# Kernel optimization log

Hardware: AMD Instinct MI355X
Metric: run time of the kernel (lower is better)

The kernel has to match this reference:

```python
import jax, jax.numpy as jnp
import numpy as np

N = 100000
E = 1600000
D = 128

def _degrees(idx, n):
    d = jax.ops.segment_sum(jnp.ones(idx.shape[0], jnp.float32), idx, num_segments=n)
    return jnp.clip(d, 1.0)

def _gconv(feat, src, dst, W, b, residual, act):
    n = feat.shape[0]
    norm_out = _degrees(src, n) ** -0.5            # [N] out-degree norm
    h = feat * norm_out[:, None]                   # scale src features
    msgs = h[src]                                  # gather [E, D]
    agg = jax.ops.segment_sum(msgs, dst, num_segments=n)  # scatter-sum [N, D]
    rst = agg @ W.T + b                            # dense linear
    norm_in = _degrees(dst, n) ** -0.5             # [N] in-degree norm
    rst = rst * norm_in[:, None]
    if residual:
        rst = rst + feat                           # identity residual (in==out)
    if act:
        rst = jax.nn.relu(rst)
    return rst

def setup_inputs() -> dict:
    key = jax.random.key(0)
    ks = jax.random.split(key, 10)
    feat = jax.random.normal(ks[0], (N, D), jnp.float32)
    src = jax.random.randint(ks[1], (E,), 0, N)
    dst = jax.random.randint(ks[2], (E,), 0, N)
    s = 1.0 / np.sqrt(D)
    W1 = jax.random.uniform(ks[3], (D, D), jnp.float32, -s, s)
    b1 = jax.random.uniform(ks[4], (D,), jnp.float32, -s, s)
    W2 = jax.random.uniform(ks[5], (D, D), jnp.float32, -s, s)
    b2 = jax.random.uniform(ks[6], (D,), jnp.float32, -s, s)
    W3 = jax.random.uniform(ks[7], (D, D), jnp.float32, -s, s)
    b3 = jax.random.uniform(ks[8], (D,), jnp.float32, -s, s)
    return {"feat": feat, "src": src, "dst": dst,
            "W1": W1, "b1": b1, "W2": W2, "b2": b2, "W3": W3, "b3": b3}

def reference(feat, src, dst, W1, b1, W2, b2, W3, b3):
    # 3-layer GCN, dropout=0, norm=None, encoding=False:
    # layers 0,1: residual + relu; layer 2: no residual, no activation
    h = _gconv(feat, src, dst, W1, b1, residual=True, act=True)
    h = _gconv(h, src, dst, W2, b2, residual=True, act=True)
    h = _gconv(h, src, dst, W3, b3, residual=False, act=False)
    return h
```

## Files before the change

### kernel.cpp

```cpp
#include <hip/hip_runtime.h>

#define NN 100000
#define EE 1600000
#define DD 128
#define NB 512
#define CAP 4608
#define CHUNK 8192

typedef __attribute__((ext_vector_type(8))) short short8v;
typedef __attribute__((ext_vector_type(4))) float f32x4;
typedef __attribute__((ext_vector_type(8))) unsigned short ushort8v;

#define LROW 136

static __device__ __forceinline__ unsigned short f2bf(float x) {
  unsigned u = __builtin_bit_cast(unsigned, x);
  return (unsigned short)((u + 0x7FFFu + ((u >> 16) & 1u)) >> 16);
}
static __device__ __forceinline__ float bf2f(unsigned short u) {
  return __builtin_bit_cast(float, (unsigned)u << 16);
}

__global__ __launch_bounds__(512) void initcur_k(int* __restrict__ cur_d,
                                                 int* __restrict__ cur_s) {
  int t = threadIdx.x;
  cur_d[t] = t * CAP;
  cur_s[t] = t * CAP;
}

__global__ __launch_bounds__(256) void split_k(const int* __restrict__ src,
                                               const int* __restrict__ dst,
                                               int* __restrict__ cur_d,
                                               int* __restrict__ cur_s,
                                               unsigned* __restrict__ tmp_d,
                                               unsigned char* __restrict__ tmp_s) {
  __shared__ int hd[NB], hs[NB], bd[NB], bs[NB];
  int t = threadIdx.x;
  int base = blockIdx.x * CHUNK;
  int end = base + CHUNK < EE ? base + CHUNK : EE;
  for (int b = t; b < NB; b += 256) { hd[b] = 0; hs[b] = 0; }
  __syncthreads();
  for (int i = base + t; i < end; i += 256) {
    atomicAdd(&hd[dst[i] >> 8], 1);
    atomicAdd(&hs[src[i] >> 8], 1);
  }
  __syncthreads();
  for (int b = t; b < NB; b += 256) {
    bd[b] = hd[b] ? atomicAdd(&cur_d[b], hd[b]) : 0;
    bs[b] = hs[b] ? atomicAdd(&cur_s[b], hs[b]) : 0;
    hd[b] = 0;
    hs[b] = 0;
  }
  __syncthreads();
  for (int i = base + t; i < end; i += 256) {
    int s = src[i];
    int d = dst[i];
    int bin = d >> 8;
    int r = atomicAdd(&hd[bin], 1);
    int pos = bd[bin] + r;
    if (pos < (bin + 1) * CAP) tmp_d[pos] = ((unsigned)(d & 255) << 17) | (unsigned)s;
    bin = s >> 8;
    r = atomicAdd(&hs[bin], 1);
    pos = bs[bin] + r;
    if (pos < (bin + 1) * CAP) tmp_s[pos] = (unsigned char)(s & 255);
  }
}

__global__ __launch_bounds__(512) void scan512_k(const int* __restrict__ cur_d,
                                                 int* __restrict__ dstart) {
  __shared__ int lds[512];
  int t = threadIdx.x;
  int v = cur_d[t] - t * CAP;
  v = v < CAP ? v : CAP;
  lds[t] = v;
  __syncthreads();
  int run = v;
  for (int off = 1; off < 512; off <<= 1) {
    int y = (t >= off) ? lds[t - off] : 0;
    __syncthreads();
    run += y;
    lds[t] = run;
    __syncthreads();
  }
  dstart[t] = run - v;
}

__global__ __launch_bounds__(256) void bucket_dst_k(const unsigned* __restrict__ tmp_d,
                                                    const int* __restrict__ cur_d,
                                                    const int* __restrict__ dstart,
                                                    int* __restrict__ csr,
                                                    int* __restrict__ row_s,
                                                    int* __restrict__ row_e,
                                                    float* __restrict__ norm_in) {
  __shared__ unsigned stage[CAP];
  __shared__ int h[256], sc[256], rk[256];
  int b = blockIdx.x;
  int t = threadIdx.x;
  int cnt = cur_d[b] - b * CAP;
  cnt = cnt < CAP ? cnt : CAP;
  int ds = dstart[b];
  for (int i = t; i < cnt; i += 256) stage[i] = tmp_d[b * CAP + i];
  h[t] = 0;
  __syncthreads();
  for (int i = t; i < cnt; i += 256) atomicAdd(&h[stage[i] >> 17], 1);
  __syncthreads();
  int v = h[t];
  sc[t] = v;
  __syncthreads();
  int run = v;
  for (int off = 1; off < 256; off <<= 1) {
    int y = (t >= off) ? sc[t - off] : 0;
    __syncthreads();
    run += y;
    sc[t] = run;
    __syncthreads();
  }
  int excl = run - v;
  int n = b * 256 + t;
  if (n < NN) {
    row_s[n] = ds + excl;
    row_e[n] = ds + excl + v;
    norm_in[n] = rsqrtf((float)(v > 1 ? v : 1));
  }
  rk[t] = excl;
  __syncthreads();
  for (int i = t; i < cnt; i += 256) {
    unsigned w = stage[i];
    int r = atomicAdd(&rk[w >> 17], 1);
    csr[ds + r] = (int)(w & 0x1FFFFu);
  }
}

__global__ __launch_bounds__(256) void bucket_src_k(const unsigned char* __restrict__ tmp_s,
                                                    const int* __restrict__ cur_s,
                                                    float* __restrict__ norm_out) {
  __shared__ int h[256];
  int b = blockIdx.x;
  int t = threadIdx.x;
  int cnt = cur_s[b] - b * CAP;
  cnt = cnt < CAP ? cnt : CAP;
  h[t] = 0;
  __syncthreads();
  const unsigned char* p = tmp_s + b * CAP;
  for (int i = t; i < cnt; i += 256) atomicAdd(&h[p[i]], 1);
  __syncthreads();
  int n = b * 256 + t;
  if (n < NN) norm_out[n] = rsqrtf((float)(h[t] > 1 ? h[t] : 1));
}

__global__ __launch_bounds__(256) void bconv_k(const float* __restrict__ w,
                                               unsigned short* __restrict__ o) {
  int i = blockIdx.x * 256 + threadIdx.x;
  float4 v = *reinterpret_cast<const float4*>(w + i * 4);
  ushort4 pk = make_ushort4(f2bf(v.x), f2bf(v.y), f2bf(v.z), f2bf(v.w));
  *reinterpret_cast<ushort4*>(o + i * 4) = pk;
}

__global__ __launch_bounds__(256) void layer_k(const unsigned short* __restrict__ h,
                                               const int* __restrict__ csr,
                                               const int* __restrict__ row_s,
                                               const int* __restrict__ row_e,
                                               const float* __restrict__ nsrc,
                                               const unsigned short* __restrict__ Wb,
                                               const float* __restrict__ bias,
                                               const float* __restrict__ nin,
                                               const float* __restrict__ residf,
                                               const unsigned short* __restrict__ residb,
                                               float* __restrict__ outf,
                                               unsigned short* __restrict__ outb,
                                               int mode) {
  __shared__ unsigned short tile[16 * LROW];
  int t = threadIdx.x;
  int n16 = t >> 4;
  int c = t & 15;
  int node = blockIdx.x * 16 + n16;

  int e0 = row_s[node];
  int e1 = row_e[node];
  float acc[8] = {0.f, 0.f, 0.f, 0.f, 0.f, 0.f, 0.f, 0.f};
  int e = e0;
  for (; e + 2 <= e1; e += 2) {
    int s0 = csr[e];
    int s1 = csr[e + 1];
    float n0 = nsrc[s0];
    float n1 = nsrc[s1];
    ushort8v u = *reinterpret_cast<const ushort8v*>(h + (size_t)s0 * DD + c * 8);
    ushort8v v = *reinterpret_cast<const ushort8v*>(h + (size_t)s1 * DD + c * 8);
#pragma unroll
    for (int i = 0; i < 8; ++i) acc[i] += bf2f(u[i]) * n0 + bf2f(v[i]) * n1;
  }
  if (e < e1) {
    int s0 = csr[e];
    float n0 = nsrc[s0];
    ushort8v u = *reinterpret_cast<const ushort8v*>(h + (size_t)s0 * DD + c * 8);
#pragma unroll
    for (int i = 0; i < 8; ++i) acc[i] += bf2f(u[i]) * n0;
  }
  ushort8v o;
#pragma unroll
  for (int i = 0; i < 8; ++i) o[i] = f2bf(acc[i]);
  *reinterpret_cast<ushort8v*>(&tile[n16 * LROW + c * 8]) = o;
  __syncthreads();

  int wid = t >> 6;
  int lane = t & 63;
  int l15 = lane & 15;
  int kgrp = lane >> 4;

  const unsigned short* bp = &tile[l15 * LROW + kgrp * 8];
  short8v b0 = *reinterpret_cast<const short8v*>(bp);
  short8v b1 = *reinterpret_cast<const short8v*>(bp + 32);
  short8v b2 = *reinterpret_cast<const short8v*>(bp + 64);
  short8v b3 = *reinterpret_cast<const short8v*>(bp + 96);

  int epnode = blockIdx.x * 16 + l15;
  float ninv = nin[epnode];

#pragma unroll
  for (int q = 0; q < 2; ++q) {
    int ct = wid * 2 + q;
    const unsigned short* wp = Wb + (size_t)(ct * 16 + l15) * DD + kgrp * 8;
    short8v w0 = *reinterpret_cast<const short8v*>(wp);
    short8v w1 = *reinterpret_cast<const short8v*>(wp + 32);
    short8v w2 = *reinterpret_cast<const short8v*>(wp + 64);
    short8v w3 = *reinterpret_cast<const short8v*>(wp + 96);
    f32x4 cacc = {0.f, 0.f, 0.f, 0.f};
    cacc = __builtin_amdgcn_mfma_f32_16x16x32_bf16(w0, b0, cacc, 0, 0, 0);
    cacc = __builtin_amdgcn_mfma_f32_16x16x32_bf16(w1, b1, cacc, 0, 0, 0);
    cacc = __builtin_amdgcn_mfma_f32_16x16x32_bf16(w2, b2, cacc, 0, 0, 0);
    cacc = __builtin_amdgcn_mfma_f32_16x16x32_bf16(w3, b3, cacc, 0, 0, 0);

    int j = ct * 16 + kgrp * 4;
    float4 bj = *reinterpret_cast<const float4*>(bias + j);
    size_t idx = (size_t)epnode * DD + j;
    float4 v;
    v.x = (cacc[0] + bj.x) * ninv;
    v.y = (cacc[1] + bj.y) * ninv;
    v.z = (cacc[2] + bj.z) * ninv;
    v.w = (cacc[3] + bj.w) * ninv;
    if (mode == 1) {
      float4 rs = *reinterpret_cast<const float4*>(residf + idx);
      v.x = fmaxf(v.x + rs.x, 0.f);
      v.y = fmaxf(v.y + rs.y, 0.f);
      v.z = fmaxf(v.z + rs.z, 0.f);
      v.w = fmaxf(v.w + rs.w, 0.f);
      ushort4 hn = make_ushort4(f2bf(v.x), f2bf(v.y), f2bf(v.z), f2bf(v.w));
      *reinterpret_cast<ushort4*>(outb + idx) = hn;
    } else if (mode == 3) {
      ushort4 rs = *reinterpret_cast<const ushort4*>(residb + idx);
      v.x = fmaxf(v.x + bf2f(rs.x), 0.f);
      v.y = fmaxf(v.y + bf2f(rs.y), 0.f);
      v.z = fmaxf(v.z + bf2f(rs.z), 0.f);
      v.w = fmaxf(v.w + bf2f(rs.w), 0.f);
      ushort4 hn = make_ushort4(f2bf(v.x), f2bf(v.y), f2bf(v.z), f2bf(v.w));
      *reinterpret_cast<ushort4*>(outb + idx) = hn;
    } else {
      *reinterpret_cast<float4*>(outf + idx) = v;
    }
  }
}

extern "C" void kernel_launch(void* const* d_in, const int* in_sizes, int n_in,
                              void* d_out, int out_size, void* d_ws, size_t ws_size,
                              hipStream_t stream) {
  const float* feat = (const float*)d_in[0];
  const int* src = (const int*)d_in[1];
  const int* dst = (const int*)d_in[2];
  const float* W1 = (const float*)d_in[3];
  const float* b1 = (const float*)d_in[4];
  const float* W2 = (const float*)d_in[5];
  const float* b2 = (const float*)d_in[6];
  const float* W3 = (const float*)d_in[7];
  const float* b3 = (const float*)d_in[8];
  float* out = (float*)d_out;

  int* row_s = (int*)d_ws;
  int* row_e = row_s + NN;
  float* norm_out = (float*)(row_e + NN);
  float* norm_in = norm_out + NN;
  int* cur_d = (int*)(norm_in + NN);
  int* cur_s = cur_d + NB;
  int* dstart = cur_s + NB;
  int* pad = dstart + NB;
  unsigned short* Wbf = (unsigned short*)pad;
  int* csr = (int*)(Wbf + 3 * 16384);
  unsigned short* vb1 = (unsigned short*)(csr + EE);
  unsigned short* vb2 = vb1 + (size_t)NN * DD;

  unsigned* tmp_d = (unsigned*)d_out;
  unsigned char* tmp_s = (unsigned char*)d_out + (size_t)NB * CAP * 4;

  initcur_k<<<1, 512, 0, stream>>>(cur_d, cur_s);
  split_k<<<(EE + CHUNK - 1) / CHUNK, 256, 0, stream>>>(src, dst, cur_d, cur_s, tmp_d, tmp_s);
  scan512_k<<<1, 512, 0, stream>>>(cur_d, dstart);
  bucket_dst_k<<<NB, 256, 0, stream>>>(tmp_d, cur_d, dstart, csr, row_s, row_e, norm_in);
  bucket_src_k<<<NB, 256, 0, stream>>>(tmp_s, cur_s, norm_out);

  bconv_k<<<16, 256, 0, stream>>>(W1, Wbf);
  bconv_k<<<16, 256, 0, stream>>>(W2, Wbf + 16384);
  bconv_k<<<16, 256, 0, stream>>>(W3, Wbf + 32768);
  bconv_k<<<12500, 256, 0, stream>>>(feat, vb1);

  layer_k<<<6250, 256, 0, stream>>>(vb1, csr, row_s, row_e, norm_out, Wbf, b1,
                                    norm_in, feat, nullptr, nullptr, vb2, 1);
  layer_k<<<6250, 256, 0, stream>>>(vb2, csr, row_s, row_e, norm_out, Wbf + 16384, b2,
                                    norm_in, nullptr, vb2, nullptr, vb1, 3);
  layer_k<<<6250, 256, 0, stream>>>(vb1, csr, row_s, row_e, norm_out, Wbf + 32768, b3,
                                    norm_in, nullptr, nullptr, out, nullptr, 0);
}
```

Baseline: 349.2 us.

## Split fused layer into XCD-sliced column aggregation and separate MFMA GEMM

Replaces the fused gather+GEMM layer kernel with two kernels. The first aggregates neighbour features one 16-column slice at a time. Each block reads its XCD id and takes work from a per-slice atomic counter, so each XCD mostly gathers one 3.2MB column slice of h, which should stay resident in that XCD's L2. The second is a standalone bf16 MFMA GEMM over a materialized aggregate buffer with the fused epilogue. This adds a full N×D bf16 write and read of the aggregate per layer, extra launches and atomic scheduling, and gathers that are now 8-byte rather than 16-byte per lane.

```diff
diff --git a/kernel.cpp b/kernel.cpp
--- a/kernel.cpp
+++ b/kernel.cpp
@@ -6,13 +6,12 @@
 #define NB 512
 #define CAP 4608
 #define CHUNK 8192
+#define NCHUNK 1563
 
 typedef __attribute__((ext_vector_type(8))) short short8v;
 typedef __attribute__((ext_vector_type(4))) float f32x4;
 typedef __attribute__((ext_vector_type(8))) unsigned short ushort8v;
 
-#define LROW 136
-
 static __device__ __forceinline__ unsigned short f2bf(float x) {
   unsigned u = __builtin_bit_cast(unsigned, x);
   return (unsigned short)((u + 0x7FFFu + ((u >> 16) & 1u)) >> 16);
@@ -22,10 +21,12 @@
 }
 
 __global__ __launch_bounds__(512) void initcur_k(int* __restrict__ cur_d,
-                                                 int* __restrict__ cur_s) {
+                                                 int* __restrict__ cur_s,
+                                                 int* __restrict__ scur) {
   int t = threadIdx.x;
   cur_d[t] = t * CAP;
   cur_s[t] = t * CAP;
+  if (t < 32) scur[t] = 0;
 }
 
 __global__ __launch_bounds__(256) void split_k(const int* __restrict__ src,
@@ -156,11 +157,68 @@
   *reinterpret_cast<ushort4*>(o + i * 4) = pk;
 }
 
-__global__ __launch_bounds__(256) void layer_k(const unsigned short* __restrict__ h,
-                                               const int* __restrict__ csr,
-                                               const int* __restrict__ row_s,
-                                               const int* __restrict__ row_e,
-                                               const float* __restrict__ nsrc,
+__global__ __launch_bounds__(256) void sliceagg_k(const unsigned short* __restrict__ h,
+                                                  const int* __restrict__ csr,
+                                                  const int* __restrict__ row_s,
+                                                  const int* __restrict__ row_e,
+                                                  const float* __restrict__ nsrc,
+                                                  int* __restrict__ scur,
+                                                  unsigned short* __restrict__ agg) {
+  __shared__ int pick_sh;
+  if (threadIdx.x == 0) {
+    unsigned xcd;
+    asm volatile("s_getreg_b32 %0, hwreg(HW_REG_XCC_ID)" : "=s"(xcd));
+    xcd &= 7u;
+    int pick = -1;
+    for (int off = 0; off < 8; ++off) {
+      int s = (int)((xcd + off) & 7u);
+      int c = atomicAdd(&scur[s], 1);
+      if (c < NCHUNK) { pick = (s << 16) | c; break; }
+    }
+    pick_sh = pick;
+  }
+  __syncthreads();
+  int pick = pick_sh;
+  if (pick < 0) return;
+  int slice = pick >> 16;
+  int chunk = pick & 0xFFFF;
+
+  int node = chunk * 64 + (threadIdx.x >> 2);
+  if (node >= NN) return;
+  int l4 = threadIdx.x & 3;
+  int colbase = slice * 16 + l4 * 4;
+
+  int e0 = row_s[node];
+  int e1 = row_e[node];
+  float a0 = 0.f, a1 = 0.f, a2 = 0.f, a3 = 0.f;
+  const unsigned short* hb = h + colbase;
+  int e = e0;
+  for (; e + 2 <= e1; e += 2) {
+    int s0 = csr[e];
+    int s1 = csr[e + 1];
+    float n0 = nsrc[s0];
+    float n1 = nsrc[s1];
+    ushort4 u = *reinterpret_cast<const ushort4*>(hb + (size_t)s0 * DD);
+    ushort4 v = *reinterpret_cast<const ushort4*>(hb + (size_t)s1 * DD);
+    a0 += bf2f(u.x) * n0 + bf2f(v.x) * n1;
+    a1 += bf2f(u.y) * n0 + bf2f(v.y) * n1;
+    a2 += bf2f(u.z) * n0 + bf2f(v.z) * n1;
+    a3 += bf2f(u.w) * n0 + bf2f(v.w) * n1;
+  }
+  if (e < e1) {
+    int s0 = csr[e];
+    float n0 = nsrc[s0];
+    ushort4 u = *reinterpret_cast<const ushort4*>(hb + (size_t)s0 * DD);
+    a0 += bf2f(u.x) * n0;
+    a1 += bf2f(u.y) * n0;
+    a2 += bf2f(u.z) * n0;
+    a3 += bf2f(u.w) * n0;
+  }
+  ushort4 o = make_ushort4(f2bf(a0), f2bf(a1), f2bf(a2), f2bf(a3));
+  *reinterpret_cast<ushort4*>(agg + (size_t)node * DD + colbase) = o;
+}
+
+__global__ __launch_bounds__(256) void gemm2_k(const unsigned short* __restrict__ A,
                                                const unsigned short* __restrict__ Wb,
                                                const float* __restrict__ bias,
                                                const float* __restrict__ nin,
@@ -169,93 +227,61 @@
                                                float* __restrict__ outf,
                                                unsigned short* __restrict__ outb,
                                                int mode) {
-  __shared__ unsigned short tile[16 * LROW];
-  int t = threadIdx.x;
-  int n16 = t >> 4;
-  int c = t & 15;
-  int node = blockIdx.x * 16 + n16;
-
-  int e0 = row_s[node];
-  int e1 = row_e[node];
-  float acc[8] = {0.f, 0.f, 0.f, 0.f, 0.f, 0.f, 0.f, 0.f};
-  int e = e0;
-  for (; e + 2 <= e1; e += 2) {
-    int s0 = csr[e];
-    int s1 = csr[e + 1];
-    float n0 = nsrc[s0];
-    float n1 = nsrc[s1];
-    ushort8v u = *reinterpret_cast<const ushort8v*>(h + (size_t)s0 * DD + c * 8);
-    ushort8v v = *reinterpret_cast<const ushort8v*>(h + (size_t)s1 * DD + c * 8);
-#pragma unroll
-    for (int i = 0; i < 8; ++i) acc[i] += bf2f(u[i]) * n0 + bf2f(v[i]) * n1;
-  }
-  if (e < e1) {
-    int s0 = csr[e];
-    float n0 = nsrc[s0];
-    ushort8v u = *reinterpret_cast<const ushort8v*>(h + (size_t)s0 * DD + c * 8);
-#pragma unroll
-    for (int i = 0; i < 8; ++i) acc[i] += bf2f(u[i]) * n0;
-  }
-  ushort8v o;
-#pragma unroll
-  for (int i = 0; i < 8; ++i) o[i] = f2bf(acc[i]);
-  *reinterpret_cast<ushort8v*>(&tile[n16 * LROW + c * 8]) = o;
-  __syncthreads();
-
-  int wid = t >> 6;
-  int lane = t & 63;
+  int wid = threadIdx.x >> 6;
+  int lane = threadIdx.x & 63;
   int l15 = lane & 15;
   int kgrp = lane >> 4;
-
-  const unsigned short* bp = &tile[l15 * LROW + kgrp * 8];
+  int node = blockIdx.x * 64 + wid * 16 + l15;
+  int nodec = node < NN ? node : NN - 1;
+
+  const unsigned short* bp = A + (size_t)nodec * DD + kgrp * 8;
   short8v b0 = *reinterpret_cast<const short8v*>(bp);
   short8v b1 = *reinterpret_cast<const short8v*>(bp + 32);
   short8v b2 = *reinterpret_cast<const short8v*>(bp + 64);
   short8v b3 = *reinterpret_cast<const short8v*>(bp + 96);
 
-  int epnode = blockIdx.x * 16 + l15;
-  float ninv = nin[epnode];
-
-#pragma unroll
-  for (int q = 0; q < 2; ++q) {
-    int ct = wid * 2 + q;
+  float ninv = nin[nodec];
+
+  for (int ct = 0; ct < 8; ++ct) {
     const unsigned short* wp = Wb + (size_t)(ct * 16 + l15) * DD + kgrp * 8;
     short8v w0 = *reinterpret_cast<const short8v*>(wp);
     short8v w1 = *reinterpret_cast<const short8v*>(wp + 32);
     short8v w2 = *reinterpret_cast<const short8v*>(wp + 64);
     short8v w3 = *reinterpret_cast<const short8v*>(wp + 96);
-    f32x4 cacc = {0.f, 0.f, 0.f, 0.f};
-    cacc = __builtin_amdgcn_mfma_f32_16x16x32_bf16(w0, b0, cacc, 0, 0, 0);
-    cacc = __builtin_amdgcn_mfma_f32_16x16x32_bf16(w1, b1, cacc, 0, 0, 0);
-    cacc = __builtin_amdgcn_mfma_f32_16x16x32_bf16(w2, b2, cacc, 0, 0, 0);
-    cacc = __builtin_amdgcn_mfma_f32_16x16x32_bf16(w3, b3, cacc, 0, 0, 0);
-
-    int j = ct * 16 + kgrp * 4;
-    float4 bj = *reinterpret_cast<const float4*>(bias + j);
-    size_t idx = (size_t)epnode * DD + j;
-    float4 v;
-    v.x = (cacc[0] + bj.x) * ninv;
-    v.y = (cacc[1] + bj.y) * ninv;
-    v.z = (cacc[2] + bj.z) * ninv;
-    v.w = (cacc[3] + bj.w) * ninv;
-    if (mode == 1) {
-      float4 rs = *reinterpret_cast<const float4*>(residf + idx);
-      v.x = fmaxf(v.x + rs.x, 0.f);
-      v.y = fmaxf(v.y + rs.y, 0.f);
-      v.z = fmaxf(v.z + rs.z, 0.f);
-      v.w = fmaxf(v.w + rs.w, 0.f);
-      ushort4 hn = make_ushort4(f2bf(v.x), f2bf(v.y), f2bf(v.z), f2bf(v.w));
-      *reinterpret_cast<ushort4*>(outb + idx) = hn;
-    } else if (mode == 3) {
-      ushort4 rs = *reinterpret_cast<const ushort4*>(residb + idx);
-      v.x = fmaxf(v.x + bf2f(rs.x), 0.f);
-      v.y = fmaxf(v.y + bf2f(rs.y), 0.f);
-      v.z = fmaxf(v.z + bf2f(rs.z), 0.f);
-      v.w = fmaxf(v.w + bf2f(rs.w), 0.f);
-      ushort4 hn = make_ushort4(f2bf(v.x), f2bf(v.y), f2bf(v.z), f2bf(v.w));
-      *reinterpret_cast<ushort4*>(outb + idx) = hn;
-    } else {
-      *reinterpret_cast<float4*>(outf + idx) = v;
+    f32x4 c = {0.f, 0.f, 0.f, 0.f};
+    c = __builtin_amdgcn_mfma_f32_16x16x32_bf16(w0, b0, c, 0, 0, 0);
+    c = __builtin_amdgcn_mfma_f32_16x16x32_bf16(w1, b1, c, 0, 0, 0);
+    c = __builtin_amdgcn_mfma_f32_16x16x32_bf16(w2, b2, c, 0, 0, 0);
+    c = __builtin_amdgcn_mfma_f32_16x16x32_bf16(w3, b3, c, 0, 0, 0);
+
+    if (node < NN) {
+      int j = ct * 16 + kgrp * 4;
+      float4 bj = *reinterpret_cast<const float4*>(bias + j);
+      size_t idx = (size_t)node * DD + j;
+      float4 v;
+      v.x = (c[0] + bj.x) * ninv;
+      v.y = (c[1] + bj.y) * ninv;
+      v.z = (c[2] + bj.z) * ninv;
+      v.w = (c[3] + bj.w) * ninv;
+      if (mode == 1) {
+        float4 rs = *reinterpret_cast<const float4*>(residf + idx);
+        v.x = fmaxf(v.x + rs.x, 0.f);
+        v.y = fmaxf(v.y + rs.y, 0.f);
+        v.z = fmaxf(v.z + rs.z, 0.f);
+        v.w = fmaxf(v.w + rs.w, 0.f);
+        ushort4 hn = make_ushort4(f2bf(v.x), f2bf(v.y), f2bf(v.z), f2bf(v.w));
+        *reinterpret_cast<ushort4*>(outb + idx) = hn;
+      } else if (mode == 3) {
+        ushort4 rs = *reinterpret_cast<const ushort4*>(residb + idx);
+        v.x = fmaxf(v.x + bf2f(rs.x), 0.f);
+        v.y = fmaxf(v.y + bf2f(rs.y), 0.f);
+        v.z = fmaxf(v.z + bf2f(rs.z), 0.f);
+        v.w = fmaxf(v.w + bf2f(rs.w), 0.f);
+        ushort4 hn = make_ushort4(f2bf(v.x), f2bf(v.y), f2bf(v.z), f2bf(v.w));
+        *reinterpret_cast<ushort4*>(outb + idx) = hn;
+      } else {
+        *reinterpret_cast<float4*>(outf + idx) = v;
+      }
     }
   }
 }
@@ -281,16 +307,17 @@
   int* cur_d = (int*)(norm_in + NN);
   int* cur_s = cur_d + NB;
   int* dstart = cur_s + NB;
-  int* pad = dstart + NB;
-  unsigned short* Wbf = (unsigned short*)pad;
+  int* scur = dstart + NB;
+  unsigned short* Wbf = (unsigned short*)(scur + 64);
   int* csr = (int*)(Wbf + 3 * 16384);
   unsigned short* vb1 = (unsigned short*)(csr + EE);
   unsigned short* vb2 = vb1 + (size_t)NN * DD;
+  unsigned short* aggb = vb2 + (size_t)NN * DD;
 
   unsigned* tmp_d = (unsigned*)d_out;
   unsigned char* tmp_s = (unsigned char*)d_out + (size_t)NB * CAP * 4;
 
-  initcur_k<<<1, 512, 0, stream>>>(cur_d, cur_s);
+  initcur_k<<<1, 512, 0, stream>>>(cur_d, cur_s, scur);
   split_k<<<(EE + CHUNK - 1) / CHUNK, 256, 0, stream>>>(src, dst, cur_d, cur_s, tmp_d, tmp_s);
   scan512_k<<<1, 512, 0, stream>>>(cur_d, dstart);
   bucket_dst_k<<<NB, 256, 0, stream>>>(tmp_d, cur_d, dstart, csr, row_s, row_e, norm_in);
@@ -301,10 +328,13 @@
   bconv_k<<<16, 256, 0, stream>>>(W3, Wbf + 32768);
   bconv_k<<<12500, 256, 0, stream>>>(feat, vb1);
 
-  layer_k<<<6250, 256, 0, stream>>>(vb1, csr, row_s, row_e, norm_out, Wbf, b1,
-                                    norm_in, feat, nullptr, nullptr, vb2, 1);
-  layer_k<<<6250, 256, 0, stream>>>(vb2, csr, row_s, row_e, norm_out, Wbf + 16384, b2,
-                                    norm_in, nullptr, vb2, nullptr, vb1, 3);
-  layer_k<<<6250, 256, 0, stream>>>(vb1, csr, row_s, row_e, norm_out, Wbf + 32768, b3,
-                                    norm_in, nullptr, nullptr, out, nullptr, 0);
-}
+  const int AB = 8 * NCHUNK;
+  const int GG = (NN + 63) / 64;
+
+  sliceagg_k<<<AB, 256, 0, stream>>>(vb1, csr, row_s, row_e, norm_out, scur, aggb);
+  gemm2_k<<<GG, 256, 0, stream>>>(aggb, Wbf, b1, norm_in, feat, nullptr, nullptr, vb2, 1);
+  sliceagg_k<<<AB, 256, 0, stream>>>(vb2, csr, row_s, row_e, norm_out, scur + 8, aggb);
+  gemm2_k<<<GG, 256, 0, stream>>>(aggb, Wbf + 16384, b2, norm_in, nullptr, vb2, nullptr, vb1, 3);
+  sliceagg_k<<<AB, 256, 0, stream>>>(vb1, csr, row_s, row_e, norm_out, scur + 16, aggb);
+  gemm2_k<<<GG, 256, 0, stream>>>(aggb, Wbf + 32768, b3, norm_in, nullptr, nullptr, out, nullptr, 0);
+}
```

Result: slower. 899.6 us (+157.6%).
